# Kernel tuning notes

Hardware: AMD Instinct MI355X
Metric: run time of the kernel (lower is better)

Reference implementation:

```python
import jax, jax.numpy as jnp
import numpy as np

N, E, D_IN, D_H, D_OUT = 100000, 1600000, 128, 128, 47
BN_EPS = 1e-5


def setup_inputs() -> dict:
    key = jax.random.key(0)
    ks = jax.random.split(key, 12)
    x = jax.random.normal(ks[0], (N, D_IN), dtype=jnp.float32)
    edge_index = jax.random.randint(ks[1], (2, E), 0, N, dtype=jnp.int64)
    s = 1.0 / np.sqrt(D_H)
    return {
        "x": x,
        "edge_index": edge_index,
        "W1": jax.random.normal(ks[2], (D_IN, D_H), dtype=jnp.float32) * s,
        "b1": jnp.zeros((D_H,), dtype=jnp.float32),
        "gamma": jax.random.uniform(ks[3], (D_H,), dtype=jnp.float32, minval=0.5, maxval=1.5),
        "beta": jax.random.normal(ks[4], (D_H,), dtype=jnp.float32) * 0.1,
        "mean": jax.random.normal(ks[5], (D_H,), dtype=jnp.float32) * 0.1,
        "var": jax.random.uniform(ks[6], (D_H,), dtype=jnp.float32, minval=0.5, maxval=1.5),
        "W2": jax.random.normal(ks[7], (D_H, D_H), dtype=jnp.float32) * s,
        "b2": jnp.zeros((D_H,), dtype=jnp.float32),
        "Wf": jax.random.normal(ks[8], (D_H, D_OUT), dtype=jnp.float32) * s,
        "bf": jnp.zeros((D_OUT,), dtype=jnp.float32),
    }


def gcn_conv(x, src, dst, W, b, n):
    # x' = x @ W, then symmetric-normalized aggregation with self-loops (PyG GCNConv).
    h = x @ W
    loops = jnp.arange(n, dtype=src.dtype)
    s = jnp.concatenate([src, loops])
    d = jnp.concatenate([dst, loops])
    deg = jax.ops.segment_sum(jnp.ones_like(d, dtype=h.dtype), d, num_segments=n)
    dinv = jnp.where(deg > 0, jax.lax.rsqrt(deg), 0.0)
    norm = dinv[s] * dinv[d]                      # [E+N]
    msg = h[s] * norm[:, None]                    # [E+N, D] gather
    out = jax.ops.segment_sum(msg, d, num_segments=n)  # scatter-add
    return out + b


def reference(x, edge_index, W1, b1, gamma, beta, mean, var, W2, b2, Wf, bf):
    n = x.shape[0]
    src, dst = edge_index[0], edge_index[1]
    # layer 1: GCNConv -> BatchNorm (eval) -> ReLU -> dropout (identity in eval)
    h1 = gcn_conv(x, src, dst, W1, b1, n)
    h1 = (h1 - mean) * jax.lax.rsqrt(var + BN_EPS) * gamma + beta
    h1 = jax.nn.relu(h1)
    # layer 2 (last conv, no BN/act)
    h2 = gcn_conv(h1, src, dst, W2, b2, n)
    # JumpingKnowledge max over layer outputs
    jk = jnp.maximum(h1, h2)
    logits = jk @ Wf + bf
    return jax.nn.log_softmax(logits, axis=1)
```

## Files before the change

### kernel.cpp

```cpp
#include <hip/hip_runtime.h>
#include <math.h>

#define DH 128
#define DOUT 47
#define BN_EPS 1e-5f

typedef __attribute__((ext_vector_type(8))) short short8;
typedef __attribute__((ext_vector_type(4))) float float4v;
typedef __attribute__((ext_vector_type(2))) float float2v;

__device__ __forceinline__ unsigned bf16_rne(float f) {
    unsigned u = __float_as_uint(f);
    return (u + 0x7fffu + ((u >> 16) & 1u)) >> 16;
}
__device__ __forceinline__ unsigned pack_bf2(float a, float b) {
    return (bf16_rne(a) & 0xffffu) | (bf16_rne(b) << 16);
}
__device__ __forceinline__ float2 unpack_bf2(unsigned u) {
    return make_float2(__uint_as_float(u << 16),
                       __uint_as_float(u & 0xffff0000u));
}

__device__ __forceinline__ void bf2_acc(float2v& a, unsigned u) {
    float2v f;
    f.x = __uint_as_float(u << 16);
    f.y = __uint_as_float(u & 0xffff0000u);
    asm("v_pk_add_f32 %0, %0, %1" : "+v"(a) : "v"(f));
}


__global__ __launch_bounds__(256) void prep_k(const float* __restrict__ W1,
                                              const float* __restrict__ W2,
                                              unsigned* __restrict__ W1b,
                                              unsigned* __restrict__ W2b,
                                              int* __restrict__ counts,
                                              unsigned* __restrict__ bufA, int n) {
    int tid = threadIdx.x;
    if (blockIdx.x >= 2) {
        int i = (blockIdx.x - 2) * 256 + tid;
        if (i < n) counts[i] = 0;
        return;
    }
    const float* W = blockIdx.x ? W2 : W1;
    unsigned* Wb = blockIdx.x ? W2b : W1b;
    if (blockIdx.x == 0 && tid < 64) bufA[(size_t)n * 64 + tid] = 0;
    for (int p = tid; p < 128 * 32; p += 256) {
        int nn = p >> 5;
        int k0 = (p & 31) << 2;
        float f0 = W[(size_t)(k0 + 0) * 128 + nn];
        float f1 = W[(size_t)(k0 + 1) * 128 + nn];
        float f2 = W[(size_t)(k0 + 2) * 128 + nn];
        float f3 = W[(size_t)(k0 + 3) * 128 + nn];
        uint2 v;
        v.x = pack_bf2(f0, f1);
        v.y = pack_bf2(f2, f3);
        *(uint2*)(Wb + (size_t)nn * 64 + (k0 >> 1)) = v;
    }
}

__global__ __launch_bounds__(256) void count_rank_k(const int* __restrict__ dst,
                                                    int* __restrict__ counts,
                                                    int* __restrict__ rank, int e) {
    int i0 = (blockIdx.x * 256 + threadIdx.x) * 8;
    if (i0 + 8 <= e) {
        int4 d4 = *(const int4*)(dst + i0);
        int4 e4 = *(const int4*)(dst + i0 + 4);
        int4 r4, s4;
        r4.x = atomicAdd(&counts[d4.x], 1);
        r4.y = atomicAdd(&counts[d4.y], 1);
        r4.z = atomicAdd(&counts[d4.z], 1);
        r4.w = atomicAdd(&counts[d4.w], 1);
        s4.x = atomicAdd(&counts[e4.x], 1);
        s4.y = atomicAdd(&counts[e4.y], 1);
        s4.z = atomicAdd(&counts[e4.z], 1);
        s4.w = atomicAdd(&counts[e4.w], 1);
        *(int4*)(rank + i0) = r4;
        *(int4*)(rank + i0 + 4) = s4;
    } else {
        for (int i = i0; i < e; i++) rank[i] = atomicAdd(&counts[dst[i]], 1);
    }
}

__global__ __launch_bounds__(256) void scan1_k(const int* __restrict__ counts,
                                               int* __restrict__ offsets,
                                               int* __restrict__ blocksums, int n) {
    __shared__ int sd[256];
    int tid = threadIdx.x;
    int base = blockIdx.x * 1024 + tid * 4;
    int v0 = (base + 0 < n) ? ((counts[base + 0] + 7) & ~7) : 0;
    int v1 = (base + 1 < n) ? ((counts[base + 1] + 7) & ~7) : 0;
    int v2 = (base + 2 < n) ? ((counts[base + 2] + 7) & ~7) : 0;
    int v3 = (base + 3 < n) ? ((counts[base + 3] + 7) & ~7) : 0;
    int tsum = v0 + v1 + v2 + v3;
    sd[tid] = tsum;
    __syncthreads();
    for (int off = 1; off < 256; off <<= 1) {
        int x = (tid >= off) ? sd[tid - off] : 0;
        __syncthreads();
        sd[tid] += x;
        __syncthreads();
    }
    if (tid == 255) blocksums[blockIdx.x] = sd[255];
    int run = sd[tid] - tsum;
    if (base + 0 < n) offsets[base + 0] = run;  run += v0;
    if (base + 1 < n) offsets[base + 1] = run;  run += v1;
    if (base + 2 < n) offsets[base + 2] = run;  run += v2;
    if (base + 3 < n) offsets[base + 3] = run;
}

__global__ __launch_bounds__(128) void scan2_k(int* __restrict__ blocksums, int nb,
                                               int* __restrict__ el, int n) {
    __shared__ int sd[128];
    int tid = threadIdx.x;
    int v = (tid < nb) ? blocksums[tid] : 0;
    sd[tid] = v;
    __syncthreads();
    for (int off = 1; off < 128; off <<= 1) {
        int x = (tid >= off) ? sd[tid - off] : 0;
        __syncthreads();
        sd[tid] += x;
        __syncthreads();
    }
    if (tid < nb) blocksums[tid] = sd[tid] - v;
    int total = sd[127];
    if (tid < 96) el[total + tid] = n;
}

__global__ void finalize_k(int* __restrict__ offsets,
                           float* __restrict__ dinv, const int* __restrict__ counts,
                           const int* __restrict__ blocksums,
                           int* __restrict__ el, int n) {
    int i = blockIdx.x * 256 + threadIdx.x;
    if (i >= n) return;
    int o = offsets[i] + blocksums[i >> 10];
    offsets[i] = o;
    int c = counts[i];
    dinv[i] = rsqrtf((float)(c + 1));
    int cP = (c + 7) & ~7;
    for (int j = o + c; j < o + cP; ++j) el[j] = n;
}

__global__ __launch_bounds__(256) void scatter_k(const int* __restrict__ src,
                                                 const int* __restrict__ dst,
                                                 const int* __restrict__ rank,
                                                 const int* __restrict__ offsets,
                                                 int* __restrict__ el, int e) {
    int i0 = (blockIdx.x * 256 + threadIdx.x) * 4;
    if (i0 + 4 <= e) {
        int4 s4 = *(const int4*)(src + i0);
        int4 d4 = *(const int4*)(dst + i0);
        int4 r4 = *(const int4*)(rank + i0);
        el[offsets[d4.x] + r4.x] = s4.x;
        el[offsets[d4.y] + r4.y] = s4.y;
        el[offsets[d4.z] + r4.z] = s4.z;
        el[offsets[d4.w] + r4.w] = s4.w;
    } else {
        for (int i = i0; i < e; i++) el[offsets[dst[i]] + rank[i]] = src[i];
    }
}

__global__ __launch_bounds__(256) void gemm_mfma_k(const float* __restrict__ A,
                                                   const unsigned* __restrict__ Wb,
                                                   const float* __restrict__ dinv,
                                                   unsigned* __restrict__ Cb, int M) {
    __shared__ ushort Bl[128 * 136];
    int tid = threadIdx.x;
    {
        unsigned* Bu = (unsigned*)Bl;
        for (int q = tid; q < 128 * 16; q += 256) {
            int row = q >> 4;
            int c = (q & 15) << 2;
            uint4 v = *(const uint4*)(Wb + (size_t)row * 64 + c);
            *(uint4*)(Bu + (size_t)row * 68 + c) = v;
        }
    }
    __syncthreads();

    int lane = tid & 63;
    int wv = tid >> 6;
    int quad = lane >> 4;
    int l15 = lane & 15;
    int r0 = blockIdx.x * 64 + wv * 16;
    int mload = r0 + l15;
    if (mload > M - 1) mload = M - 1;
    const float* Ar = A + (size_t)mload * 128 + quad * 8;

    float4v acc[8];
#pragma unroll
    for (int t = 0; t < 8; t++) acc[t] = (float4v){0.f, 0.f, 0.f, 0.f};

    for (int kp = 0; kp < 4; ++kp) {
        float4 a0 = *(const float4*)(Ar + kp * 32);
        float4 a1 = *(const float4*)(Ar + kp * 32 + 4);
        float af[8] = {a0.x, a0.y, a0.z, a0.w, a1.x, a1.y, a1.z, a1.w};
        short8 av;
#pragma unroll
        for (int j = 0; j < 8; j++) av[j] = (short)bf16_rne(af[j]);
        int kb = kp * 32 + quad * 8;
#pragma unroll
        for (int nt = 0; nt < 8; nt++) {
            short8 b8 = *(const short8*)(&Bl[(size_t)(nt * 16 + l15) * 136 + kb]);
            acc[nt] = __builtin_amdgcn_mfma_f32_16x16x32_bf16(av, b8, acc[nt], 0, 0, 0);
        }
    }

    ushort* Cu = (ushort*)Cb;
#pragma unroll
    for (int r = 0; r < 4; r++) {
        int row = r0 + quad * 4 + r;
        if (row < M) {
            float dv = dinv[row];
#pragma unroll
            for (int nt = 0; nt < 8; nt++) {
                Cu[(size_t)row * 128 + nt * 16 + l15] =
                    (ushort)bf16_rne(acc[nt][r] * dv);
            }
        }
    }
}

__global__ __launch_bounds__(256) void gemm_bf16_k(const unsigned* __restrict__ Ab,
                                                   const unsigned* __restrict__ Wb,
                                                   const float* __restrict__ dinv,
                                                   unsigned* __restrict__ Cb, int M) {
    __shared__ ushort Bl[128 * 136];
    int tid = threadIdx.x;
    {
        unsigned* Bu = (unsigned*)Bl;
        for (int q = tid; q < 128 * 16; q += 256) {
            int row = q >> 4;
            int c = (q & 15) << 2;
            uint4 v = *(const uint4*)(Wb + (size_t)row * 64 + c);
            *(uint4*)(Bu + (size_t)row * 68 + c) = v;
        }
    }
    __syncthreads();

    int lane = tid & 63;
    int wv = tid >> 6;
    int quad = lane >> 4;
    int l15 = lane & 15;
    int r0 = blockIdx.x * 64 + wv * 16;
    int mload = r0 + l15;
    if (mload > M - 1) mload = M - 1;
    const unsigned* Ar = Ab + (size_t)mload * 64 + quad * 4;

    float4v acc[8];
#pragma unroll
    for (int t = 0; t < 8; t++) acc[t] = (float4v){0.f, 0.f, 0.f, 0.f};

    for (int kp = 0; kp < 4; ++kp) {
        uint4 a4 = *(const uint4*)(Ar + kp * 16);
        short8 av;
        av[0] = (short)(a4.x & 0xffff); av[1] = (short)(a4.x >> 16);
        av[2] = (short)(a4.y & 0xffff); av[3] = (short)(a4.y >> 16);
        av[4] = (short)(a4.z & 0xffff); av[5] = (short)(a4.z >> 16);
        av[6] = (short)(a4.w & 0xffff); av[7] = (short)(a4.w >> 16);
        int kb = kp * 32 + quad * 8;
#pragma unroll
        for (int nt = 0; nt < 8; nt++) {
            short8 b8 = *(const short8*)(&Bl[(size_t)(nt * 16 + l15) * 136 + kb]);
            acc[nt] = __builtin_amdgcn_mfma_f32_16x16x32_bf16(av, b8, acc[nt], 0, 0, 0);
        }
    }

    ushort* Cu = (ushort*)Cb;
#pragma unroll
    for (int r = 0; r < 4; r++) {
        int row = r0 + quad * 4 + r;
        if (row < M) {
            float dv = dinv[row];
#pragma unroll
            for (int nt = 0; nt < 8; nt++) {
                Cu[(size_t)row * 128 + nt * 16 + l15] =
                    (ushort)bf16_rne(acc[nt][r] * dv);
            }
        }
    }
}

__device__ __forceinline__ float4 agg_core(const uint2* __restrict__ Hu2,
                                           const int* __restrict__ el,
                                           int start, int cnt, int node,
                                           int li, int half) {
    float2v a01 = {0.f, 0.f};
    float2v a23 = {0.f, 0.f};
    int groups = ((cnt + 7) & ~7) >> 3;
    if (groups > 0) {
        const int* p = el + start + half * 4;
        int4 r = *(const int4*)p;
        uint2 c0 = Hu2[(size_t)r.x * 32 + li];
        uint2 c1 = Hu2[(size_t)r.y * 32 + li];
        uint2 c2 = Hu2[(size_t)r.z * 32 + li];
        uint2 c3 = Hu2[(size_t)r.w * 32 + li];
        int4 rn = *(const int4*)(p + 8);
        for (int g = 0; g < groups; ++g) {
            uint2 n0 = Hu2[(size_t)rn.x * 32 + li];
            uint2 n1 = Hu2[(size_t)rn.y * 32 + li];
            uint2 n2 = Hu2[(size_t)rn.z * 32 + li];
            uint2 n3 = Hu2[(size_t)rn.w * 32 + li];
            int4 r2 = *(const int4*)(p + 8 * (g + 2));
            bf2_acc(a01, c0.x); bf2_acc(a23, c0.y);
            bf2_acc(a01, c1.x); bf2_acc(a23, c1.y);
            bf2_acc(a01, c2.x); bf2_acc(a23, c2.y);
            bf2_acc(a01, c3.x); bf2_acc(a23, c3.y);
            c0 = n0; c1 = n1; c2 = n2; c3 = n3;
            rn = r2;
        }
    }
    float4 acc = make_float4(a01.x, a01.y, a23.x, a23.y);
    acc.x += __shfl_xor(acc.x, 32);
    acc.y += __shfl_xor(acc.y, 32);
    acc.z += __shfl_xor(acc.z, 32);
    acc.w += __shfl_xor(acc.w, 32);
    uint2 sv = Hu2[(size_t)node * 32 + li];
    float2 s0 = unpack_bf2(sv.x);
    float2 s1 = unpack_bf2(sv.y);
    acc.x += s0.x; acc.y += s0.y; acc.z += s1.x; acc.w += s1.y;
    return acc;
}

__global__ __launch_bounds__(256) void agg1_k(
    const unsigned* __restrict__ H, const int* __restrict__ el,
    const int* __restrict__ offsets, const int* __restrict__ counts,
    const float* __restrict__ dinv, const float* __restrict__ b1,
    const float* __restrict__ gamma, const float* __restrict__ beta,
    const float* __restrict__ mean, const float* __restrict__ var,
    unsigned* __restrict__ H1b, int n) {
    int lane = threadIdx.x & 63;
    int li = lane & 31;
    int half = lane >> 5;
    int node = blockIdx.x * 4 + (threadIdx.x >> 6);
    if (node >= n) return;
    float4 acc = agg_core((const uint2*)H, el, offsets[node], counts[node],
                          node, li, half);
    if (half == 0) {
        float dv = dinv[node];
        int f0 = li * 4;
        float4 bb = *(const float4*)(b1 + f0);
        float4 mm = *(const float4*)(mean + f0);
        float4 vv = *(const float4*)(var + f0);
        float4 gg = *(const float4*)(gamma + f0);
        float4 be = *(const float4*)(beta + f0);
        float4 o;
        o.x = fmaxf((acc.x * dv + bb.x - mm.x) * rsqrtf(vv.x + BN_EPS) * gg.x + be.x, 0.f);
        o.y = fmaxf((acc.y * dv + bb.y - mm.y) * rsqrtf(vv.y + BN_EPS) * gg.y + be.y, 0.f);
        o.z = fmaxf((acc.z * dv + bb.z - mm.z) * rsqrtf(vv.z + BN_EPS) * gg.z + be.z, 0.f);
        o.w = fmaxf((acc.w * dv + bb.w - mm.w) * rsqrtf(vv.w + BN_EPS) * gg.w + be.w, 0.f);
        uint2 pk;
        pk.x = pack_bf2(o.x, o.y);
        pk.y = pack_bf2(o.z, o.w);
        *(uint2*)(H1b + (size_t)node * 64 + li * 2) = pk;
    }
}

__global__ __launch_bounds__(256) void agg2_k(
    const unsigned* __restrict__ H, const int* __restrict__ el,
    const int* __restrict__ offsets, const int* __restrict__ counts,
    const float* __restrict__ dinv, const float* __restrict__ b2,
    unsigned* __restrict__ H1b, int n) {
    int lane = threadIdx.x & 63;
    int li = lane & 31;
    int half = lane >> 5;
    int node = blockIdx.x * 4 + (threadIdx.x >> 6);
    if (node >= n) return;
    float4 acc = agg_core((const uint2*)H, el, offsets[node], counts[node],
                          node, li, half);
    if (half == 0) {
        float dv = dinv[node];
        int f0 = li * 4;
        float4 bb = *(const float4*)(b2 + f0);
        uint2* p = (uint2*)(H1b + (size_t)node * 64 + li * 2);
        uint2 hv = *p;
        float2 ha = unpack_bf2(hv.x);
        float2 hb = unpack_bf2(hv.y);
        float4 o;
        o.x = fmaxf(ha.x, acc.x * dv + bb.x);
        o.y = fmaxf(ha.y, acc.y * dv + bb.y);
        o.z = fmaxf(hb.x, acc.z * dv + bb.z);
        o.w = fmaxf(hb.y, acc.w * dv + bb.w);
        uint2 pk;
        pk.x = pack_bf2(o.x, o.y);
        pk.y = pack_bf2(o.z, o.w);
        *p = pk;
    }
}

__global__ __launch_bounds__(256) void head_k(const unsigned* __restrict__ JKb,
                                              const float* __restrict__ Wf,
                                              const float* __restrict__ bf,
                                              float* __restrict__ out, int n) {
    __shared__ __align__(16) float Bs[48 * 132];
    __shared__ __align__(16) float As[64 * 36];
    int tid = threadIdx.x;
    for (int p = tid; p < 47 * 32; p += 256) {
        int c = p >> 5;
        int k0 = (p & 31) << 2;
        float4 v;
        v.x = Wf[(size_t)(k0 + 0) * DOUT + c];
        v.y = Wf[(size_t)(k0 + 1) * DOUT + c];
        v.z = Wf[(size_t)(k0 + 2) * DOUT + c];
        v.w = Wf[(size_t)(k0 + 3) * DOUT + c];
        *(float4*)(&Bs[c * 132 + k0]) = v;
    }
    int tx = tid & 15;
    int ty = tid >> 4;
    int node0 = blockIdx.x * 64;

    float acc[4][3];
#pragma unroll
    for (int i = 0; i < 4; i++)
#pragma unroll
        for (int j = 0; j < 3; j++) acc[i][j] = 0.f;

    for (int kk = 0; kk < 128; kk += 32) {
        __syncthreads();
        for (int l = tid; l < 512; l += 256) {
            int r = l >> 3;
            int c4 = (l & 7) << 2;
            int row = node0 + r;
            float4 v = make_float4(0.f, 0.f, 0.f, 0.f);
            if (row < n) {
                uint2 u = *(const uint2*)(JKb + (size_t)row * 64 + ((kk + c4) >> 1));
                float2 f0 = unpack_bf2(u.x);
                float2 f1 = unpack_bf2(u.y);
                v = make_float4(f0.x, f0.y, f1.x, f1.y);
            }
            *(float4*)(&As[r * 36 + c4]) = v;
        }
        __syncthreads();
#pragma unroll
        for (int k4 = 0; k4 < 32; k4 += 4) {
            float4 a0 = *(const float4*)(&As[(ty * 4 + 0) * 36 + k4]);
            float4 a1 = *(const float4*)(&As[(ty * 4 + 1) * 36 + k4]);
            float4 a2 = *(const float4*)(&As[(ty * 4 + 2) * 36 + k4]);
            float4 a3 = *(const float4*)(&As[(ty * 4 + 3) * 36 + k4]);
            float4 b0 = *(const float4*)(&Bs[(tx * 3 + 0) * 132 + kk + k4]);
            float4 b1 = *(const float4*)(&Bs[(tx * 3 + 1) * 132 + kk + k4]);
            float4 b2 = *(const float4*)(&Bs[(tx * 3 + 2) * 132 + kk + k4]);
#define DOT_ROW(i, a)                                                        \
            acc[i][0] = fmaf(a.x, b0.x, acc[i][0]);                          \
            acc[i][0] = fmaf(a.y, b0.y, acc[i][0]);                          \
            acc[i][0] = fmaf(a.z, b0.z, acc[i][0]);                          \
            acc[i][0] = fmaf(a.w, b0.w, acc[i][0]);                          \
            acc[i][1] = fmaf(a.x, b1.x, acc[i][1]);                          \
            acc[i][1] = fmaf(a.y, b1.y, acc[i][1]);                          \
            acc[i][1] = fmaf(a.z, b1.z, acc[i][1]);                          \
            acc[i][1] = fmaf(a.w, b1.w, acc[i][1]);                          \
            acc[i][2] = fmaf(a.x, b2.x, acc[i][2]);                          \
            acc[i][2] = fmaf(a.y, b2.y, acc[i][2]);                          \
            acc[i][2] = fmaf(a.z, b2.z, acc[i][2]);                          \
            acc[i][2] = fmaf(a.w, b2.w, acc[i][2]);
            DOT_ROW(0, a0)
            DOT_ROW(1, a1)
            DOT_ROW(2, a2)
            DOT_ROW(3, a3)
#undef DOT_ROW
        }
    }

    float bfv[3];
#pragma unroll
    for (int j = 0; j < 3; j++) {
        int c = tx * 3 + j;
        bfv[j] = (c < DOUT) ? bf[c] : 0.f;
    }
#pragma unroll
    for (int i = 0; i < 4; i++) {
        int node = node0 + ty * 4 + i;
        float l0 = acc[i][0] + bfv[0];
        float l1 = acc[i][1] + bfv[1];
        float l2 = acc[i][2] + bfv[2];
        bool v2ok = (tx * 3 + 2) < DOUT;
        float m = fmaxf(l0, l1);
        if (v2ok) m = fmaxf(m, l2);
        for (int off = 8; off >= 1; off >>= 1) m = fmaxf(m, __shfl_xor(m, off));
        float s = expf(l0 - m) + expf(l1 - m) + (v2ok ? expf(l2 - m) : 0.f);
        for (int off = 8; off >= 1; off >>= 1) s += __shfl_xor(s, off);
        float ls = m + logf(s);
        if (node < n) {
            float* o = out + (size_t)node * DOUT + tx * 3;
            o[0] = l0 - ls;
            o[1] = l1 - ls;
            if (v2ok) o[2] = l2 - ls;
        }
    }
}

extern "C" void kernel_launch(void* const* d_in, const int* in_sizes, int n_in,
                              void* d_out, int out_size, void* d_ws, size_t ws_size,
                              hipStream_t stream) {
    const float* x     = (const float*)d_in[0];
    const int*   ei    = (const int*)d_in[1];
    const float* W1    = (const float*)d_in[2];
    const float* b1    = (const float*)d_in[3];
    const float* gamma = (const float*)d_in[4];
    const float* beta  = (const float*)d_in[5];
    const float* mean  = (const float*)d_in[6];
    const float* var   = (const float*)d_in[7];
    const float* W2    = (const float*)d_in[8];
    const float* b2    = (const float*)d_in[9];
    const float* Wf    = (const float*)d_in[10];
    const float* bf    = (const float*)d_in[11];
    float* out = (float*)d_out;

    int N_ = in_sizes[0] / 128;
    int E_ = in_sizes[1] / 2;
    const int* src = ei;
    const int* dst = ei + E_;

    char* ws = (char*)d_ws;
    unsigned* bufA = (unsigned*)ws; ws += (size_t)(N_ + 1) * 64 * 4;
    unsigned* h1b  = (unsigned*)ws; ws += (size_t)N_ * 64 * 4;
    int*   counts  = (int*)ws;    ws += (size_t)N_ * 4;
    int*   offsets = (int*)ws;    ws += (size_t)N_ * 4;
    float* dinv    = (float*)ws;  ws += (size_t)N_ * 4;
    int*   rank    = (int*)ws;    ws += (size_t)E_ * 4;
    int*   el      = (int*)ws;    ws += ((size_t)E_ + 7 * (size_t)N_ + 128) * 4;
    int*   bsums   = (int*)ws;    ws += 1024 * 4;
    unsigned* W1b  = (unsigned*)ws; ws += 128 * 64 * 4;
    unsigned* W2b  = (unsigned*)ws; ws += 128 * 64 * 4;

    int nb = (N_ + 1023) / 1024;
    int gemmBlocks = (N_ + 63) / 64;
    int edgeBlocks8 = (E_ + 2047) / 2048;
    int edgeBlocks = (E_ + 1023) / 1024;

    prep_k<<<2 + (N_ + 255) / 256, 256, 0, stream>>>(W1, W2, W1b, W2b,
                                                     counts, bufA, N_);
    count_rank_k<<<edgeBlocks8, 256, 0, stream>>>(dst, counts, rank, E_);
    scan1_k<<<nb, 256, 0, stream>>>(counts, offsets, bsums, N_);
    scan2_k<<<1, 128, 0, stream>>>(bsums, nb, el, N_);
    finalize_k<<<(N_ + 255) / 256, 256, 0, stream>>>(offsets, dinv,
                                                     counts, bsums, el, N_);
    scatter_k<<<edgeBlocks, 256, 0, stream>>>(src, dst, rank, offsets, el, E_);

    gemm_mfma_k<<<gemmBlocks, 256, 0, stream>>>(x, W1b, dinv, bufA, N_);
    agg1_k<<<(N_ + 3) / 4, 256, 0, stream>>>(bufA, el, offsets, counts, dinv,
                                             b1, gamma, beta, mean, var, h1b, N_);
    gemm_bf16_k<<<gemmBlocks, 256, 0, stream>>>(h1b, W2b, dinv, bufA, N_);
    agg2_k<<<(N_ + 3) / 4, 256, 0, stream>>>(bufA, el, offsets, counts, dinv,
                                             b2, h1b, N_);
    head_k<<<(N_ + 63) / 64, 256, 0, stream>>>(h1b, Wf, bf, out, N_);
}
```

Before: 421.2 us.

## Fuse first GEMM with degree counting and pack quantized source norm into edge list

The layer-1 GEMM no longer depends on dinv, so it now runs in the same launch as the atomic degree counting, with blocks interleaved two GEMM to one count. The per-row dinv scaling after each GEMM is dropped. Instead, each edge-list entry packs a 15-bit quantized dinv[src] into the upper bits of the source index, and the aggregation applies it with an FMA. The self-loop term is scaled by the node's own dinv. Degree counters are padded to one per 64-byte line to reduce atomic contention. In exchange, the norm is quantized to 15 bits, node ids are limited to 17 bits, and the counter array is 16x larger.

```diff
diff --git a/kernel.cpp b/kernel.cpp
--- a/kernel.cpp
+++ b/kernel.cpp
@@ -19,13 +19,6 @@
 __device__ __forceinline__ float2 unpack_bf2(unsigned u) {
     return make_float2(__uint_as_float(u << 16),
                        __uint_as_float(u & 0xffff0000u));
-}
-
-__device__ __forceinline__ void bf2_acc(float2v& a, unsigned u) {
-    float2v f;
-    f.x = __uint_as_float(u << 16);
-    f.y = __uint_as_float(u & 0xffff0000u);
-    asm("v_pk_add_f32 %0, %0, %1" : "+v"(a) : "v"(f));
 }
 
 
@@ -33,12 +26,12 @@
                                               const float* __restrict__ W2,
                                               unsigned* __restrict__ W1b,
                                               unsigned* __restrict__ W2b,
-                                              int* __restrict__ counts,
+                                              int* __restrict__ countsP,
                                               unsigned* __restrict__ bufA, int n) {
     int tid = threadIdx.x;
     if (blockIdx.x >= 2) {
-        int i = (blockIdx.x - 2) * 256 + tid;
-        if (i < n) counts[i] = 0;
+        int i4 = (blockIdx.x - 2) * 256 + tid;
+        if (i4 < n * 4) *(int4*)(countsP + (size_t)i4 * 4) = make_int4(0, 0, 0, 0);
         return;
     }
     const float* W = blockIdx.x ? W2 : W1;
@@ -58,39 +51,105 @@
     }
 }
 
-__global__ __launch_bounds__(256) void count_rank_k(const int* __restrict__ dst,
-                                                    int* __restrict__ counts,
-                                                    int* __restrict__ rank, int e) {
-    int i0 = (blockIdx.x * 256 + threadIdx.x) * 8;
-    if (i0 + 8 <= e) {
-        int4 d4 = *(const int4*)(dst + i0);
-        int4 e4 = *(const int4*)(dst + i0 + 4);
-        int4 r4, s4;
-        r4.x = atomicAdd(&counts[d4.x], 1);
-        r4.y = atomicAdd(&counts[d4.y], 1);
-        r4.z = atomicAdd(&counts[d4.z], 1);
-        r4.w = atomicAdd(&counts[d4.w], 1);
-        s4.x = atomicAdd(&counts[e4.x], 1);
-        s4.y = atomicAdd(&counts[e4.y], 1);
-        s4.z = atomicAdd(&counts[e4.z], 1);
-        s4.w = atomicAdd(&counts[e4.w], 1);
-        *(int4*)(rank + i0) = r4;
-        *(int4*)(rank + i0 + 4) = s4;
-    } else {
-        for (int i = i0; i < e; i++) rank[i] = atomicAdd(&counts[dst[i]], 1);
-    }
-}
-
-__global__ __launch_bounds__(256) void scan1_k(const int* __restrict__ counts,
+__global__ __launch_bounds__(256) void fused_gc_k(
+    const float* __restrict__ A, const unsigned* __restrict__ Wb,
+    unsigned* __restrict__ Cb, int M,
+    const int* __restrict__ dst, int* __restrict__ countsP,
+    int* __restrict__ rank, int e, int gemmBlocks) {
+    __shared__ ushort Bl[128 * 136];
+    int bid = blockIdx.x;
+    int r3 = bid % 3;
+    int q3 = bid / 3;
+    int tid = threadIdx.x;
+
+    if (r3 == 2) {
+        int i0 = (q3 * 256 + tid) * 8;
+        if (i0 + 8 <= e) {
+            int4 d4 = *(const int4*)(dst + i0);
+            int4 e4 = *(const int4*)(dst + i0 + 4);
+            int4 r4, s4;
+            r4.x = atomicAdd(&countsP[(size_t)d4.x * 16], 1);
+            r4.y = atomicAdd(&countsP[(size_t)d4.y * 16], 1);
+            r4.z = atomicAdd(&countsP[(size_t)d4.z * 16], 1);
+            r4.w = atomicAdd(&countsP[(size_t)d4.w * 16], 1);
+            s4.x = atomicAdd(&countsP[(size_t)e4.x * 16], 1);
+            s4.y = atomicAdd(&countsP[(size_t)e4.y * 16], 1);
+            s4.z = atomicAdd(&countsP[(size_t)e4.z * 16], 1);
+            s4.w = atomicAdd(&countsP[(size_t)e4.w * 16], 1);
+            *(int4*)(rank + i0) = r4;
+            *(int4*)(rank + i0 + 4) = s4;
+        } else {
+            for (int i = i0; i < e; i++)
+                rank[i] = atomicAdd(&countsP[(size_t)dst[i] * 16], 1);
+        }
+        return;
+    }
+
+    int gIdx = q3 * 2 + r3;
+    if (gIdx >= gemmBlocks) return;
+    {
+        unsigned* Bu = (unsigned*)Bl;
+        for (int q = tid; q < 128 * 16; q += 256) {
+            int row = q >> 4;
+            int c = (q & 15) << 2;
+            uint4 v = *(const uint4*)(Wb + (size_t)row * 64 + c);
+            *(uint4*)(Bu + (size_t)row * 68 + c) = v;
+        }
+    }
+    __syncthreads();
+
+    int lane = tid & 63;
+    int wv = tid >> 6;
+    int quad = lane >> 4;
+    int l15 = lane & 15;
+    int r0 = gIdx * 64 + wv * 16;
+    int mload = r0 + l15;
+    if (mload > M - 1) mload = M - 1;
+    const float* Ar = A + (size_t)mload * 128 + quad * 8;
+
+    float4v acc[8];
+#pragma unroll
+    for (int t = 0; t < 8; t++) acc[t] = (float4v){0.f, 0.f, 0.f, 0.f};
+
+    for (int kp = 0; kp < 4; ++kp) {
+        float4 a0 = *(const float4*)(Ar + kp * 32);
+        float4 a1 = *(const float4*)(Ar + kp * 32 + 4);
+        float af[8] = {a0.x, a0.y, a0.z, a0.w, a1.x, a1.y, a1.z, a1.w};
+        short8 av;
+#pragma unroll
+        for (int j = 0; j < 8; j++) av[j] = (short)bf16_rne(af[j]);
+        int kb = kp * 32 + quad * 8;
+#pragma unroll
+        for (int nt = 0; nt < 8; nt++) {
+            short8 b8 = *(const short8*)(&Bl[(size_t)(nt * 16 + l15) * 136 + kb]);
+            acc[nt] = __builtin_amdgcn_mfma_f32_16x16x32_bf16(av, b8, acc[nt], 0, 0, 0);
+        }
+    }
+
+    ushort* Cu = (ushort*)Cb;
+#pragma unroll
+    for (int r = 0; r < 4; r++) {
+        int row = r0 + quad * 4 + r;
+        if (row < M) {
+#pragma unroll
+            for (int nt = 0; nt < 8; nt++) {
+                Cu[(size_t)row * 128 + nt * 16 + l15] =
+                    (ushort)bf16_rne(acc[nt][r]);
+            }
+        }
+    }
+}
+
+__global__ __launch_bounds__(256) void scan1_k(const int* __restrict__ countsP,
                                                int* __restrict__ offsets,
                                                int* __restrict__ blocksums, int n) {
     __shared__ int sd[256];
     int tid = threadIdx.x;
     int base = blockIdx.x * 1024 + tid * 4;
-    int v0 = (base + 0 < n) ? ((counts[base + 0] + 7) & ~7) : 0;
-    int v1 = (base + 1 < n) ? ((counts[base + 1] + 7) & ~7) : 0;
-    int v2 = (base + 2 < n) ? ((counts[base + 2] + 7) & ~7) : 0;
-    int v3 = (base + 3 < n) ? ((counts[base + 3] + 7) & ~7) : 0;
+    int v0 = (base + 0 < n) ? ((countsP[(size_t)(base + 0) * 16] + 7) & ~7) : 0;
+    int v1 = (base + 1 < n) ? ((countsP[(size_t)(base + 1) * 16] + 7) & ~7) : 0;
+    int v2 = (base + 2 < n) ? ((countsP[(size_t)(base + 2) * 16] + 7) & ~7) : 0;
+    int v3 = (base + 3 < n) ? ((countsP[(size_t)(base + 3) * 16] + 7) & ~7) : 0;
     int tsum = v0 + v1 + v2 + v3;
     sd[tid] = tsum;
     __syncthreads();
@@ -127,14 +186,14 @@
 }
 
 __global__ void finalize_k(int* __restrict__ offsets,
-                           float* __restrict__ dinv, const int* __restrict__ counts,
+                           float* __restrict__ dinv, const int* __restrict__ countsP,
                            const int* __restrict__ blocksums,
                            int* __restrict__ el, int n) {
     int i = blockIdx.x * 256 + threadIdx.x;
     if (i >= n) return;
     int o = offsets[i] + blocksums[i >> 10];
     offsets[i] = o;
-    int c = counts[i];
+    int c = countsP[(size_t)i * 16];
     dinv[i] = rsqrtf((float)(c + 1));
     int cP = (c + 7) & ~7;
     for (int j = o + c; j < o + cP; ++j) el[j] = n;
@@ -144,24 +203,31 @@
                                                  const int* __restrict__ dst,
                                                  const int* __restrict__ rank,
                                                  const int* __restrict__ offsets,
+                                                 const float* __restrict__ dinv,
                                                  int* __restrict__ el, int e) {
     int i0 = (blockIdx.x * 256 + threadIdx.x) * 4;
     if (i0 + 4 <= e) {
         int4 s4 = *(const int4*)(src + i0);
         int4 d4 = *(const int4*)(dst + i0);
         int4 r4 = *(const int4*)(rank + i0);
-        el[offsets[d4.x] + r4.x] = s4.x;
-        el[offsets[d4.y] + r4.y] = s4.y;
-        el[offsets[d4.z] + r4.z] = s4.z;
-        el[offsets[d4.w] + r4.w] = s4.w;
+        unsigned qx = (unsigned)(dinv[s4.x] * 32767.f + 0.5f);
+        unsigned qy = (unsigned)(dinv[s4.y] * 32767.f + 0.5f);
+        unsigned qz = (unsigned)(dinv[s4.z] * 32767.f + 0.5f);
+        unsigned qw = (unsigned)(dinv[s4.w] * 32767.f + 0.5f);
+        el[offsets[d4.x] + r4.x] = (int)((unsigned)s4.x | (qx << 17));
+        el[offsets[d4.y] + r4.y] = (int)((unsigned)s4.y | (qy << 17));
+        el[offsets[d4.z] + r4.z] = (int)((unsigned)s4.z | (qz << 17));
+        el[offsets[d4.w] + r4.w] = (int)((unsigned)s4.w | (qw << 17));
     } else {
-        for (int i = i0; i < e; i++) el[offsets[dst[i]] + rank[i]] = src[i];
-    }
-}
-
-__global__ __launch_bounds__(256) void gemm_mfma_k(const float* __restrict__ A,
+        for (int i = i0; i < e; i++) {
+            unsigned q = (unsigned)(dinv[src[i]] * 32767.f + 0.5f);
+            el[offsets[dst[i]] + rank[i]] = (int)((unsigned)src[i] | (q << 17));
+        }
+    }
+}
+
+__global__ __launch_bounds__(256) void gemm_bf16_k(const unsigned* __restrict__ Ab,
                                                    const unsigned* __restrict__ Wb,
-                                                   const float* __restrict__ dinv,
                                                    unsigned* __restrict__ Cb, int M) {
     __shared__ ushort Bl[128 * 136];
     int tid = threadIdx.x;
@@ -183,66 +249,6 @@
     int r0 = blockIdx.x * 64 + wv * 16;
     int mload = r0 + l15;
     if (mload > M - 1) mload = M - 1;
-    const float* Ar = A + (size_t)mload * 128 + quad * 8;
-
-    float4v acc[8];
-#pragma unroll
-    for (int t = 0; t < 8; t++) acc[t] = (float4v){0.f, 0.f, 0.f, 0.f};
-
-    for (int kp = 0; kp < 4; ++kp) {
-        float4 a0 = *(const float4*)(Ar + kp * 32);
-        float4 a1 = *(const float4*)(Ar + kp * 32 + 4);
-        float af[8] = {a0.x, a0.y, a0.z, a0.w, a1.x, a1.y, a1.z, a1.w};
-        short8 av;
-#pragma unroll
-        for (int j = 0; j < 8; j++) av[j] = (short)bf16_rne(af[j]);
-        int kb = kp * 32 + quad * 8;
-#pragma unroll
-        for (int nt = 0; nt < 8; nt++) {
-            short8 b8 = *(const short8*)(&Bl[(size_t)(nt * 16 + l15) * 136 + kb]);
-            acc[nt] = __builtin_amdgcn_mfma_f32_16x16x32_bf16(av, b8, acc[nt], 0, 0, 0);
-        }
-    }
-
-    ushort* Cu = (ushort*)Cb;
-#pragma unroll
-    for (int r = 0; r < 4; r++) {
-        int row = r0 + quad * 4 + r;
-        if (row < M) {
-            float dv = dinv[row];
-#pragma unroll
-            for (int nt = 0; nt < 8; nt++) {
-                Cu[(size_t)row * 128 + nt * 16 + l15] =
-                    (ushort)bf16_rne(acc[nt][r] * dv);
-            }
-        }
-    }
-}
-
-__global__ __launch_bounds__(256) void gemm_bf16_k(const unsigned* __restrict__ Ab,
-                                                   const unsigned* __restrict__ Wb,
-                                                   const float* __restrict__ dinv,
-                                                   unsigned* __restrict__ Cb, int M) {
-    __shared__ ushort Bl[128 * 136];
-    int tid = threadIdx.x;
-    {
-        unsigned* Bu = (unsigned*)Bl;
-        for (int q = tid; q < 128 * 16; q += 256) {
-            int row = q >> 4;
-            int c = (q & 15) << 2;
-            uint4 v = *(const uint4*)(Wb + (size_t)row * 64 + c);
-            *(uint4*)(Bu + (size_t)row * 68 + c) = v;
-        }
-    }
-    __syncthreads();
-
-    int lane = tid & 63;
-    int wv = tid >> 6;
-    int quad = lane >> 4;
-    int l15 = lane & 15;
-    int r0 = blockIdx.x * 64 + wv * 16;
-    int mload = r0 + l15;
-    if (mload > M - 1) mload = M - 1;
     const unsigned* Ar = Ab + (size_t)mload * 64 + quad * 4;
 
     float4v acc[8];
@@ -269,11 +275,10 @@
     for (int r = 0; r < 4; r++) {
         int row = r0 + quad * 4 + r;
         if (row < M) {
-            float dv = dinv[row];
 #pragma unroll
             for (int nt = 0; nt < 8; nt++) {
                 Cu[(size_t)row * 128 + nt * 16 + l15] =
-                    (ushort)bf16_rne(acc[nt][r] * dv);
+                    (ushort)bf16_rne(acc[nt][r]);
             }
         }
     }
@@ -282,31 +287,40 @@
 __device__ __forceinline__ float4 agg_core(const uint2* __restrict__ Hu2,
                                            const int* __restrict__ el,
                                            int start, int cnt, int node,
-                                           int li, int half) {
+                                           float dvn, int li, int half) {
     float2v a01 = {0.f, 0.f};
     float2v a23 = {0.f, 0.f};
     int groups = ((cnt + 7) & ~7) >> 3;
     if (groups > 0) {
         const int* p = el + start + half * 4;
-        int4 r = *(const int4*)p;
-        uint2 c0 = Hu2[(size_t)r.x * 32 + li];
-        uint2 c1 = Hu2[(size_t)r.y * 32 + li];
-        uint2 c2 = Hu2[(size_t)r.z * 32 + li];
-        uint2 c3 = Hu2[(size_t)r.w * 32 + li];
+
+#define EDGE(cu, rr) {                                                       \
+        float qf = (float)((unsigned)(rr) >> 17) * (1.f / 32767.f);          \
+        float2v f0, f1;                                                      \
+        f0.x = __uint_as_float((cu).x << 16);                                \
+        f0.y = __uint_as_float((cu).x & 0xffff0000u);                        \
+        f1.x = __uint_as_float((cu).y << 16);                                \
+        f1.y = __uint_as_float((cu).y & 0xffff0000u);                        \
+        a01.x = fmaf(f0.x, qf, a01.x); a01.y = fmaf(f0.y, qf, a01.y);        \
+        a23.x = fmaf(f1.x, qf, a23.x); a23.y = fmaf(f1.y, qf, a23.y);        \
+}
+        int4 rc = *(const int4*)p;
+        uint2 c0 = Hu2[(size_t)(rc.x & 0x1FFFF) * 32 + li];
+        uint2 c1 = Hu2[(size_t)(rc.y & 0x1FFFF) * 32 + li];
+        uint2 c2 = Hu2[(size_t)(rc.z & 0x1FFFF) * 32 + li];
+        uint2 c3 = Hu2[(size_t)(rc.w & 0x1FFFF) * 32 + li];
         int4 rn = *(const int4*)(p + 8);
         for (int g = 0; g < groups; ++g) {
-            uint2 n0 = Hu2[(size_t)rn.x * 32 + li];
-            uint2 n1 = Hu2[(size_t)rn.y * 32 + li];
-            uint2 n2 = Hu2[(size_t)rn.z * 32 + li];
-            uint2 n3 = Hu2[(size_t)rn.w * 32 + li];
+            uint2 n0 = Hu2[(size_t)(rn.x & 0x1FFFF) * 32 + li];
+            uint2 n1 = Hu2[(size_t)(rn.y & 0x1FFFF) * 32 + li];
+            uint2 n2 = Hu2[(size_t)(rn.z & 0x1FFFF) * 32 + li];
+            uint2 n3 = Hu2[(size_t)(rn.w & 0x1FFFF) * 32 + li];
             int4 r2 = *(const int4*)(p + 8 * (g + 2));
-            bf2_acc(a01, c0.x); bf2_acc(a23, c0.y);
-            bf2_acc(a01, c1.x); bf2_acc(a23, c1.y);
-            bf2_acc(a01, c2.x); bf2_acc(a23, c2.y);
-            bf2_acc(a01, c3.x); bf2_acc(a23, c3.y);
+            EDGE(c0, rc.x) EDGE(c1, rc.y) EDGE(c2, rc.z) EDGE(c3, rc.w)
             c0 = n0; c1 = n1; c2 = n2; c3 = n3;
-            rn = r2;
-        }
+            rc = rn; rn = r2;
+        }
+#undef EDGE
     }
     float4 acc = make_float4(a01.x, a01.y, a23.x, a23.y);
     acc.x += __shfl_xor(acc.x, 32);
@@ -316,7 +330,8 @@
     uint2 sv = Hu2[(size_t)node * 32 + li];
     float2 s0 = unpack_bf2(sv.x);
     float2 s1 = unpack_bf2(sv.y);
-    acc.x += s0.x; acc.y += s0.y; acc.z += s1.x; acc.w += s1.y;
+    acc.x = fmaf(s0.x, dvn, acc.x); acc.y = fmaf(s0.y, dvn, acc.y);
+    acc.z = fmaf(s1.x, dvn, acc.z); acc.w = fmaf(s1.y, dvn, acc.w);
     return acc;
 }
 
@@ -332,10 +347,10 @@
     int half = lane >> 5;
     int node = blockIdx.x * 4 + (threadIdx.x >> 6);
     if (node >= n) return;
-    float4 acc = agg_core((const uint2*)H, el, offsets[node], counts[node],
-                          node, li, half);
+    float dv = dinv[node];
+    float4 acc = agg_core((const uint2*)H, el, offsets[node],
+                          counts[(size_t)node * 16], node, dv, li, half);
     if (half == 0) {
-        float dv = dinv[node];
         int f0 = li * 4;
         float4 bb = *(const float4*)(b1 + f0);
         float4 mm = *(const float4*)(mean + f0);
@@ -364,10 +379,10 @@
     int half = lane >> 5;
     int node = blockIdx.x * 4 + (threadIdx.x >> 6);
     if (node >= n) return;
-    float4 acc = agg_core((const uint2*)H, el, offsets[node], counts[node],
-                          node, li, half);
+    float dv = dinv[node];
+    float4 acc = agg_core((const uint2*)H, el, offsets[node],
+                          counts[(size_t)node * 16], node, dv, li, half);
     if (half == 0) {
-        float dv = dinv[node];
         int f0 = li * 4;
         float4 bb = *(const float4*)(b2 + f0);
         uint2* p = (uint2*)(H1b + (size_t)node * 64 + li * 2);
@@ -512,7 +527,7 @@
     char* ws = (char*)d_ws;
     unsigned* bufA = (unsigned*)ws; ws += (size_t)(N_ + 1) * 64 * 4;
     unsigned* h1b  = (unsigned*)ws; ws += (size_t)N_ * 64 * 4;
-    int*   counts  = (int*)ws;    ws += (size_t)N_ * 4;
+    int* countsP   = (int*)ws;    ws += (size_t)N_ * 16 * 4;
     int*   offsets = (int*)ws;    ws += (size_t)N_ * 4;
     float* dinv    = (float*)ws;  ws += (size_t)N_ * 4;
     int*   rank    = (int*)ws;    ws += (size_t)E_ * 4;
@@ -523,23 +538,25 @@
 
     int nb = (N_ + 1023) / 1024;
     int gemmBlocks = (N_ + 63) / 64;
-    int edgeBlocks8 = (E_ + 2047) / 2048;
+    int countBlocks = (E_ + 2047) / 2048;
+    int pairs = countBlocks > (gemmBlocks + 1) / 2 ? countBlocks : (gemmBlocks + 1) / 2;
+    int fusedGrid = 3 * pairs;
     int edgeBlocks = (E_ + 1023) / 1024;
-
-    prep_k<<<2 + (N_ + 255) / 256, 256, 0, stream>>>(W1, W2, W1b, W2b,
-                                                     counts, bufA, N_);
-    count_rank_k<<<edgeBlocks8, 256, 0, stream>>>(dst, counts, rank, E_);
-    scan1_k<<<nb, 256, 0, stream>>>(counts, offsets, bsums, N_);
+    int zeroBlocks = (N_ * 4 + 255) / 256;
+
+    prep_k<<<2 + zeroBlocks, 256, 0, stream>>>(W1, W2, W1b, W2b, countsP, bufA, N_);
+    fused_gc_k<<<fusedGrid, 256, 0, stream>>>(x, W1b, bufA, N_,
+                                              dst, countsP, rank, E_, gemmBlocks);
+    scan1_k<<<nb, 256, 0, stream>>>(countsP, offsets, bsums, N_);
     scan2_k<<<1, 128, 0, stream>>>(bsums, nb, el, N_);
     finalize_k<<<(N_ + 255) / 256, 256, 0, stream>>>(offsets, dinv,
-                                                     counts, bsums, el, N_);
-    scatter_k<<<edgeBlocks, 256, 0, stream>>>(src, dst, rank, offsets, el, E_);
-
-    gemm_mfma_k<<<gemmBlocks, 256, 0, stream>>>(x, W1b, dinv, bufA, N_);
-    agg1_k<<<(N_ + 3) / 4, 256, 0, stream>>>(bufA, el, offsets, counts, dinv,
+                                                     countsP, bsums, el, N_);
+    scatter_k<<<edgeBlocks, 256, 0, stream>>>(src, dst, rank, offsets, dinv, el, E_);
+
+    agg1_k<<<(N_ + 3) / 4, 256, 0, stream>>>(bufA, el, offsets, countsP, dinv,
                                              b1, gamma, beta, mean, var, h1b, N_);
-    gemm_bf16_k<<<gemmBlocks, 256, 0, stream>>>(h1b, W2b, dinv, bufA, N_);
-    agg2_k<<<(N_ + 3) / 4, 256, 0, stream>>>(bufA, el, offsets, counts, dinv,
+    gemm_bf16_k<<<gemmBlocks, 256, 0, stream>>>(h1b, W2b, bufA, N_);
+    agg2_k<<<(N_ + 3) / 4, 256, 0, stream>>>(bufA, el, offsets, countsP, dinv,
                                              b2, h1b, N_);
     head_k<<<(N_ + 63) / 64, 256, 0, stream>>>(h1b, Wf, bf, out, N_);
 }
```

After: 414.2 us. No clear change (-1.7%).
